# Performance work log

Hardware: AMD Instinct MI355X
Metric: run time of the kernel (lower is better)

## Reference

```python
import math
import jax, jax.numpy as jnp
import numpy as np

K = 4            # ensemble size
S_CONST = 0.25   # isotropic gaussian scale constant
GAUSS_DIM = 6

def pixel_shuffle(x, r):
    B, C, H, W = x.shape
    C2 = C // (r * r)
    x = x.reshape(B, C2, r, r, H, W).transpose(0, 1, 4, 2, 5, 3)
    return x.reshape(B, C2, H * r, W * r)

def pixel_unshuffle(x, r):
    B, C, H, W = x.shape
    x = x.reshape(B, C, H // r, r, W // r, r).transpose(0, 1, 3, 5, 2, 4)
    return x.reshape(B, C * r * r, H // r, W // r)

def setup_inputs():
    key = jax.random.key(0)
    k1, k2, k3 = jax.random.split(key, 3)
    B, h, w = 4, 128, 128
    inp = jax.random.normal(k1, (B, 3, h, w), jnp.float32)
    w_enc = jax.random.normal(k2, (1024, 3, 3, 3), jnp.float32) * 0.05
    b_enc = jnp.zeros((1024,), jnp.float32)
    w_head = jax.random.normal(k3, (GAUSS_DIM * K, 256), jnp.float32) * 0.05
    b_head = jnp.zeros((GAUSS_DIM * K,), jnp.float32)
    return {"inp": inp, "w_enc": w_enc, "b_enc": b_enc,
            "w_head": w_head, "b_head": b_head, "scale": 2}

def _forward(inp, w_enc, b_enc, w_head, b_head, scale):
    B, _, h, w = inp.shape
    s1 = s2 = float(scale)
    H, W = round(h * s1), round(w * s2)
    # --- encoder (conv3x3 -> pixel_shuffle x4 -> 64ch @ 4h x 4w) ---
    x = jax.lax.conv_general_dilated(inp, w_enc, (1, 1), 'SAME',
        dimension_numbers=('NCHW', 'OIHW', 'NCHW')) + b_enc[None, :, None, None]
    x = pixel_shuffle(x, 4)                 # [B, 64, 4h, 4w]
    feat = pixel_unshuffle(x, 2)            # [B, 256, 2h, 2w]
    # --- gauss head (1x1 conv) ---
    pred_map = jnp.einsum('bchw,oc->bohw', feat, w_head) + b_head[None, :, None, None]
    gh, gw = 2 * h, 2 * w
    N = gh * gw
    pred = pred_map.reshape(B, GAUSS_DIM * K, N).transpose(0, 2, 1).reshape(B, N, K, GAUSS_DIM)
    rgb_k, off_raw, w_logits = pred[..., :3], pred[..., 3:5], pred[..., 5:6]
    wgt = jax.nn.softmax(w_logits, axis=2)
    rgb = (rgb_k * wgt).sum(2)              # [B, N, 3]
    off = (jnp.tanh(off_raw) * wgt).sum(2)  # [B, N, 2]
    # --- gaussian centers in NDC ---
    yi, xi = jnp.meshgrid(jnp.arange(gh), jnp.arange(gw), indexing='ij')
    coordx = (xi / gw * 2.0 - 1.0).reshape(-1).astype(jnp.float32)
    coordy = (yi / gh * 2.0 - 1.0).reshape(-1).astype(jnp.float32)
    x_ndc = coordx[None, :] + 2.0 * off[..., 0] / w - 1.0 / W
    y_ndc = coordy[None, :] + 2.0 * off[..., 1] / h - 1.0 / H
    # --- rasterize: isotropic gaussians, local 3-sigma window, scatter-add ---
    s_px = S_CONST * s1                     # pixel-space std (theta = 0)
    r = max(2, int(math.ceil(3.0 * s_px)))
    offs = jnp.arange(-r, r + 1)

    def raster_one(xn, yn, col):
        cx = 0.5 * ((xn + 1.0) * W - 1.0)   # ndc -> pixel center
        cy = 0.5 * ((yn + 1.0) * H - 1.0)
        px = jnp.floor(cx)[:, None] + offs  # [N, 2r+1]
        py = jnp.floor(cy)[:, None] + offs
        dx = px - cx[:, None]
        dy = py - cy[:, None]
        power = -0.5 * (dy[:, :, None] ** 2 + dx[:, None, :] ** 2) / (s_px * s_px)
        alpha = jnp.minimum(0.999, jnp.exp(power))
        alpha = jnp.where(alpha > 1.0 / 255.0, alpha, 0.0)   # kernel alpha cutoff
        pxi = px.astype(jnp.int32)
        pyi = py.astype(jnp.int32)
        valid = ((pyi[:, :, None] >= 0) & (pyi[:, :, None] < H) &
                 (pxi[:, None, :] >= 0) & (pxi[:, None, :] < W))
        contrib = jnp.where(valid, alpha, 0.0)               # [N, wy, wx]
        yfull = jnp.clip(jnp.broadcast_to(pyi[:, :, None], contrib.shape), 0, H - 1)
        xfull = jnp.clip(jnp.broadcast_to(pxi[:, None, :], contrib.shape), 0, W - 1)
        img = jnp.zeros((H, W, 3), jnp.float32).at[yfull, xfull].add(
            contrib[..., None] * col[:, None, None, :])
        return jnp.clip(img, 0.0, 1.0).transpose(2, 0, 1)    # [3, H, W]

    return jax.vmap(raster_one)(x_ndc, y_ndc, rgb)

def reference(inp, w_enc, b_enc, w_head, b_head, scale):
    return _forward(inp, w_enc, b_enc, w_head, b_head, scale)
```

## Files before the change

### kernel.cpp

```cpp
#include <hip/hip_runtime.h>
#include <math.h>

#define NB 4
#define IH 128
#define IW 128
#define GH 256
#define GW 256
#define NGAUSS (NB * GH * GW)

#define WEFF_FLOATS (4 * 24 * 27)
#define BEFF_FLOATS (4 * 24)
#define POS_OFF 2688
#define COL_OFF (POS_OFF + 2 * NGAUSS)

#define TSX 16
#define TSY 16
#define GR 22
#define NREG (GR * GR)
#define RR_MAX 2.770360f
#define EXP2C (-2.8853900818f)

__device__ __forceinline__ float fast_tanh(float x) {
  return 1.f - 2.f / (__expf(2.f * x) + 1.f);
}
__device__ __forceinline__ float clamp01(float v) {
  return fminf(1.f, fmaxf(0.f, v));
}

__global__ __launch_bounds__(256) void weff_kernel(
    const float* __restrict__ w_enc, const float* __restrict__ b_enc,
    const float* __restrict__ w_head, const float* __restrict__ b_head,
    float* __restrict__ weff, float* __restrict__ beff) {
  __shared__ float sWH[24 * 256];
  __shared__ float sWE[256 * 27];
  __shared__ float sBE[256];

  int tid = (int)threadIdx.x;
  int p = (int)blockIdx.x;
  int ph = p >> 1, pw = p & 1;

  for (int i = tid; i < 24 * 256; i += 256) sWH[i] = w_head[i];
  {
    int hc = tid;
    int ch = ((hc >> 2) << 4) + (2 * ph + ((hc >> 1) & 1)) * 4 + (2 * pw + (hc & 1));
    for (int t = 0; t < 27; ++t) sWE[hc * 27 + t] = w_enc[ch * 27 + t];
    sBE[hc] = b_enc[ch];
  }
  __syncthreads();

  for (int j = tid; j < 24 * 27; j += 256) {
    int o = j / 27, t = j % 27;
    float a = 0.f;
    for (int hc = 0; hc < 256; ++hc) a = fmaf(sWH[o * 256 + hc], sWE[hc * 27 + t], a);
    weff[p * (24 * 27) + j] = a;
  }
  if (tid < 24) {
    float a = b_head[tid];
    for (int hc = 0; hc < 256; ++hc) a = fmaf(sWH[tid * 256 + hc], sBE[hc], a);
    beff[p * 24 + tid] = a;
  }
}

__global__ __launch_bounds__(256, 4) void gauss_kernel(
    const float* __restrict__ inp, const float* __restrict__ ws_ro,
    float* __restrict__ ws) {
  __shared__ float sW[4 * 24 * 28];
  __shared__ float sB[BEFF_FLOATS];

  int tid = (int)threadIdx.x;
  for (int i = tid; i < 4 * 24 * 28; i += 256) {
    int row = i / 28, k = i - row * 28;
    sW[i] = (k < 27) ? ws_ro[row * 27 + k] : 0.f;
  }
  for (int i = tid; i < BEFF_FLOATS; i += 256) sB[i] = ws_ro[WEFF_FLOATS + i];
  __syncthreads();

  int bid = (int)blockIdx.x;
  int b = bid >> 8;
  int t = bid & 255;
  int hh = (t >> 4) * 16 + (tid >> 4);
  int ww = (t & 15) * 16 + (tid & 15);
  int p = (hh & 1) * 2 + (ww & 1);
  int hs = hh >> 1, ws_ = ww >> 1;

  const float* ib = inp + b * 3 * IH * IW;
  float in[28];
  in[27] = 0.f;
  #pragma unroll
  for (int cin = 0; cin < 3; ++cin) {
    #pragma unroll
    for (int ky = 0; ky < 3; ++ky) {
      int y = hs + ky - 1;
      bool yok = (y >= 0 && y < IH);
      #pragma unroll
      for (int kx = 0; kx < 3; ++kx) {
        int x = ws_ + kx - 1;
        float v = 0.f;
        if (yok && x >= 0 && x < IW) v = ib[(cin * IH + y) * IW + x];
        in[cin * 9 + ky * 3 + kx] = v;
      }
    }
  }

  float pr[24];
  #pragma unroll
  for (int o = 0; o < 24; ++o) {
    float a = sB[p * 24 + o];
    const float4* wrow = (const float4*)&sW[(p * 24 + o) * 28];
    #pragma unroll
    for (int kq = 0; kq < 7; ++kq) {
      float4 w = wrow[kq];
      a = fmaf(in[kq * 4 + 0], w.x, a);
      a = fmaf(in[kq * 4 + 1], w.y, a);
      a = fmaf(in[kq * 4 + 2], w.z, a);
      a = fmaf(in[kq * 4 + 3], w.w, a);
    }
    pr[o] = a;
  }

  float l0 = pr[5], l1 = pr[11], l2 = pr[17], l3 = pr[23];
  float m = fmaxf(fmaxf(l0, l1), fmaxf(l2, l3));
  float e0 = __expf(l0 - m), e1 = __expf(l1 - m);
  float e2 = __expf(l2 - m), e3 = __expf(l3 - m);
  float inv = 1.f / (e0 + e1 + e2 + e3);
  float w0 = e0 * inv, w1 = e1 * inv, w2 = e2 * inv, w3 = e3 * inv;
  float cr = w0 * pr[0] + w1 * pr[6] + w2 * pr[12] + w3 * pr[18];
  float cg = w0 * pr[1] + w1 * pr[7] + w2 * pr[13] + w3 * pr[19];
  float cb = w0 * pr[2] + w1 * pr[8] + w2 * pr[14] + w3 * pr[20];
  float ox = w0 * fast_tanh(pr[3]) + w1 * fast_tanh(pr[9]) +
             w2 * fast_tanh(pr[15]) + w3 * fast_tanh(pr[21]);
  float oy = w0 * fast_tanh(pr[4]) + w1 * fast_tanh(pr[10]) +
             w2 * fast_tanh(pr[16]) + w3 * fast_tanh(pr[22]);

  float coordx = ((float)ww / 256.f) * 2.f - 1.f;
  float coordy = ((float)hh / 256.f) * 2.f - 1.f;
  float x_ndc = coordx + 2.f * ox / 128.f - 1.f / 256.f;
  float y_ndc = coordy + 2.f * oy / 128.f - 1.f / 256.f;
  float cx = 0.5f * ((x_ndc + 1.f) * 256.f - 1.f);
  float cy = 0.5f * ((y_ndc + 1.f) * 256.f - 1.f);

  int g = (b << 16) | (hh << 8) | ww;
  ((float2*)(ws + POS_OFF))[g] = make_float2(cy, cx);
  ((float4*)(ws + COL_OFF))[g] = make_float4(cr, cg, cb, 0.f);
}

__global__ __launch_bounds__(256, 4) void gather_kernel(
    const float* __restrict__ ws, float* __restrict__ out) {
  __shared__ float2 sPos[NREG];
  __shared__ float4 sCol[NREG];

  int tid = (int)threadIdx.x;
  int bid = (int)blockIdx.x;
  int b = bid >> 8;
  int t = bid & 255;
  int TY = (t >> 4) * TSY;
  int TX = (t & 15) * TSX;
  const float2* posP = (const float2*)(ws + POS_OFF);
  const float4* colP = (const float4*)(ws + COL_OFF);

  for (int i = tid; i < NREG; i += 256) {
    int r = i / GR, c = i - r * GR;
    int hh = TY - 2 + r, ww = TX - 2 + c;
    if ((unsigned)hh < GH && (unsigned)ww < GW) {
      int g = (b << 16) | (hh << 8) | ww;
      sPos[i] = posP[g];
      sCol[i] = colP[g];
    } else {
      sPos[i] = make_float2(1e9f, 1e9f);
      sCol[i] = make_float4(0.f, 0.f, 0.f, 0.f);
    }
  }
  __syncthreads();

  int pxl = tid & 15, pyl = tid >> 4;
  float fpx = (float)(TX + pxl), fpy = (float)(TY + pyl);
  float ar = 0.f, ag = 0.f, ab = 0.f;

  #pragma unroll
  for (int ry = 0; ry < 7; ++ry) {
    int base = (pyl + ry) * GR + pxl;
    #pragma unroll
    for (int rx = 0; rx < 7; ++rx) {
      float2 P = sPos[base + rx];
      float dy = fpy - P.x;
      float dx = fpx - P.y;
      float rr = fmaf(dy, dy, dx * dx);
      if (rr < RR_MAX) {
        float al = fminf(0.999f, exp2f(EXP2C * rr));
        float4 C = sCol[base + rx];
        ar = fmaf(al, C.x, ar);
        ag = fmaf(al, C.y, ag);
        ab = fmaf(al, C.z, ab);
      }
    }
  }

  float* ob = out + b * 3 * GH * GW;
  int i0 = (TY + pyl) * GW + (TX + pxl);
  ob[i0] = clamp01(ar);
  ob[GH * GW + i0] = clamp01(ag);
  ob[2 * GH * GW + i0] = clamp01(ab);
}

extern "C" void kernel_launch(void* const* d_in, const int* in_sizes, int n_in,
                              void* d_out, int out_size, void* d_ws, size_t ws_size,
                              hipStream_t stream) {
  const float* inp = (const float*)d_in[0];
  const float* w_enc = (const float*)d_in[1];
  const float* b_enc = (const float*)d_in[2];
  const float* w_head = (const float*)d_in[3];
  const float* b_head = (const float*)d_in[4];

  float* ws = (float*)d_ws;
  float* weff = ws;
  float* beff = ws + WEFF_FLOATS;

  weff_kernel<<<4, 256, 0, stream>>>(w_enc, b_enc, w_head, b_head, weff, beff);

  gauss_kernel<<<NB * 256, 256, 0, stream>>>(inp, ws, ws);

  gather_kernel<<<NB * 256, 256, 0, stream>>>(ws, (float*)d_out);
}
```

Baseline: 112.9 us.

## Fuse gaussian prediction into rasterization kernel with halo recomputation

Merges the per-pixel gaussian parameter kernel into the gather/raster kernel. Each tile stages its input patch in shared memory and recomputes the gaussians for its 22x22 halo region directly into shared memory, one parity class per wave. This removes the global workspace round trip for positions and colors and one kernel launch. In exchange it roughly doubles the gaussian compute through halo recomputation, and lanes are partly idle in the second iteration.

```diff
diff --git a/kernel.cpp b/kernel.cpp
--- a/kernel.cpp
+++ b/kernel.cpp
@@ -6,12 +6,9 @@
 #define IW 128
 #define GH 256
 #define GW 256
-#define NGAUSS (NB * GH * GW)
 
 #define WEFF_FLOATS (4 * 24 * 27)
 #define BEFF_FLOATS (4 * 24)
-#define POS_OFF 2688
-#define COL_OFF (POS_OFF + 2 * NGAUSS)
 
 #define TSX 16
 #define TSY 16
@@ -19,6 +16,9 @@
 #define NREG (GR * GR)
 #define RR_MAX 2.770360f
 #define EXP2C (-2.8853900818f)
+
+#define IPS 13
+#define IPSP 14
 
 __device__ __forceinline__ float fast_tanh(float x) {
   return 1.f - 2.f / (__expf(2.f * x) + 1.f);
@@ -61,91 +61,12 @@
   }
 }
 
-__global__ __launch_bounds__(256, 4) void gauss_kernel(
+__global__ __launch_bounds__(256, 4) void render_kernel(
     const float* __restrict__ inp, const float* __restrict__ ws_ro,
-    float* __restrict__ ws) {
+    float* __restrict__ out) {
   __shared__ float sW[4 * 24 * 28];
   __shared__ float sB[BEFF_FLOATS];
-
-  int tid = (int)threadIdx.x;
-  for (int i = tid; i < 4 * 24 * 28; i += 256) {
-    int row = i / 28, k = i - row * 28;
-    sW[i] = (k < 27) ? ws_ro[row * 27 + k] : 0.f;
-  }
-  for (int i = tid; i < BEFF_FLOATS; i += 256) sB[i] = ws_ro[WEFF_FLOATS + i];
-  __syncthreads();
-
-  int bid = (int)blockIdx.x;
-  int b = bid >> 8;
-  int t = bid & 255;
-  int hh = (t >> 4) * 16 + (tid >> 4);
-  int ww = (t & 15) * 16 + (tid & 15);
-  int p = (hh & 1) * 2 + (ww & 1);
-  int hs = hh >> 1, ws_ = ww >> 1;
-
-  const float* ib = inp + b * 3 * IH * IW;
-  float in[28];
-  in[27] = 0.f;
-  #pragma unroll
-  for (int cin = 0; cin < 3; ++cin) {
-    #pragma unroll
-    for (int ky = 0; ky < 3; ++ky) {
-      int y = hs + ky - 1;
-      bool yok = (y >= 0 && y < IH);
-      #pragma unroll
-      for (int kx = 0; kx < 3; ++kx) {
-        int x = ws_ + kx - 1;
-        float v = 0.f;
-        if (yok && x >= 0 && x < IW) v = ib[(cin * IH + y) * IW + x];
-        in[cin * 9 + ky * 3 + kx] = v;
-      }
-    }
-  }
-
-  float pr[24];
-  #pragma unroll
-  for (int o = 0; o < 24; ++o) {
-    float a = sB[p * 24 + o];
-    const float4* wrow = (const float4*)&sW[(p * 24 + o) * 28];
-    #pragma unroll
-    for (int kq = 0; kq < 7; ++kq) {
-      float4 w = wrow[kq];
-      a = fmaf(in[kq * 4 + 0], w.x, a);
-      a = fmaf(in[kq * 4 + 1], w.y, a);
-      a = fmaf(in[kq * 4 + 2], w.z, a);
-      a = fmaf(in[kq * 4 + 3], w.w, a);
-    }
-    pr[o] = a;
-  }
-
-  float l0 = pr[5], l1 = pr[11], l2 = pr[17], l3 = pr[23];
-  float m = fmaxf(fmaxf(l0, l1), fmaxf(l2, l3));
-  float e0 = __expf(l0 - m), e1 = __expf(l1 - m);
-  float e2 = __expf(l2 - m), e3 = __expf(l3 - m);
-  float inv = 1.f / (e0 + e1 + e2 + e3);
-  float w0 = e0 * inv, w1 = e1 * inv, w2 = e2 * inv, w3 = e3 * inv;
-  float cr = w0 * pr[0] + w1 * pr[6] + w2 * pr[12] + w3 * pr[18];
-  float cg = w0 * pr[1] + w1 * pr[7] + w2 * pr[13] + w3 * pr[19];
-  float cb = w0 * pr[2] + w1 * pr[8] + w2 * pr[14] + w3 * pr[20];
-  float ox = w0 * fast_tanh(pr[3]) + w1 * fast_tanh(pr[9]) +
-             w2 * fast_tanh(pr[15]) + w3 * fast_tanh(pr[21]);
-  float oy = w0 * fast_tanh(pr[4]) + w1 * fast_tanh(pr[10]) +
-             w2 * fast_tanh(pr[16]) + w3 * fast_tanh(pr[22]);
-
-  float coordx = ((float)ww / 256.f) * 2.f - 1.f;
-  float coordy = ((float)hh / 256.f) * 2.f - 1.f;
-  float x_ndc = coordx + 2.f * ox / 128.f - 1.f / 256.f;
-  float y_ndc = coordy + 2.f * oy / 128.f - 1.f / 256.f;
-  float cx = 0.5f * ((x_ndc + 1.f) * 256.f - 1.f);
-  float cy = 0.5f * ((y_ndc + 1.f) * 256.f - 1.f);
-
-  int g = (b << 16) | (hh << 8) | ww;
-  ((float2*)(ws + POS_OFF))[g] = make_float2(cy, cx);
-  ((float4*)(ws + COL_OFF))[g] = make_float4(cr, cg, cb, 0.f);
-}
-
-__global__ __launch_bounds__(256, 4) void gather_kernel(
-    const float* __restrict__ ws, float* __restrict__ out) {
+  __shared__ float sIn[3 * IPS * IPSP];
   __shared__ float2 sPos[NREG];
   __shared__ float4 sCol[NREG];
 
@@ -155,19 +76,97 @@
   int t = bid & 255;
   int TY = (t >> 4) * TSY;
   int TX = (t & 15) * TSX;
-  const float2* posP = (const float2*)(ws + POS_OFF);
-  const float4* colP = (const float4*)(ws + COL_OFF);
-
-  for (int i = tid; i < NREG; i += 256) {
-    int r = i / GR, c = i - r * GR;
-    int hh = TY - 2 + r, ww = TX - 2 + c;
-    if ((unsigned)hh < GH && (unsigned)ww < GW) {
-      int g = (b << 16) | (hh << 8) | ww;
-      sPos[i] = posP[g];
-      sCol[i] = colP[g];
-    } else {
-      sPos[i] = make_float2(1e9f, 1e9f);
-      sCol[i] = make_float4(0.f, 0.f, 0.f, 0.f);
+
+  for (int i = tid; i < 4 * 24 * 28; i += 256) {
+    int row = i / 28, k = i - row * 28;
+    sW[i] = (k < 27) ? ws_ro[row * 27 + k] : 0.f;
+  }
+  for (int i = tid; i < BEFF_FLOATS; i += 256) sB[i] = ws_ro[WEFF_FLOATS + i];
+
+  {
+    const float* ib = inp + b * 3 * IH * IW;
+    int y0 = (TY >> 1) - 2, x0 = (TX >> 1) - 2;
+    for (int i = tid; i < 3 * IPS * IPSP; i += 256) {
+      int c = i / (IPS * IPSP);
+      int r = i - c * (IPS * IPSP);
+      int ry = r / IPSP, rx = r - ry * IPSP;
+      float v = 0.f;
+      int y = y0 + ry, x = x0 + rx;
+      if (rx < IPS && y >= 0 && y < IH && x >= 0 && x < IW)
+        v = ib[(c * IH + y) * IW + x];
+      sIn[i] = v;
+    }
+  }
+  __syncthreads();
+
+  {
+    int wave = tid >> 6;
+    int lane = tid & 63;
+    int ph = wave >> 1, pw = wave & 1;
+    for (int j = lane; j < 121; j += 64) {
+      int qy = j / 11, qx = j - qy * 11;
+      int gyr = 2 * qy + ph, gxr = 2 * qx + pw;
+      int gi = gyr * GR + gxr;
+      int hh = TY - 2 + gyr, ww = TX - 2 + gxr;
+
+      if ((unsigned)hh < GH && (unsigned)ww < GW) {
+        float in[28];
+        in[27] = 0.f;
+        #pragma unroll
+        for (int cin = 0; cin < 3; ++cin) {
+          #pragma unroll
+          for (int ky = 0; ky < 3; ++ky) {
+            int rr_ = (qy + ky) * IPSP + qx;
+            #pragma unroll
+            for (int kx = 0; kx < 3; ++kx) {
+              in[cin * 9 + ky * 3 + kx] = sIn[cin * IPS * IPSP + rr_ + kx];
+            }
+          }
+        }
+
+        float pr[24];
+        #pragma unroll
+        for (int o = 0; o < 24; ++o) {
+          float a = sB[wave * 24 + o];
+          const float4* wrow = (const float4*)&sW[(wave * 24 + o) * 28];
+          #pragma unroll
+          for (int kq = 0; kq < 7; ++kq) {
+            float4 w = wrow[kq];
+            a = fmaf(in[kq * 4 + 0], w.x, a);
+            a = fmaf(in[kq * 4 + 1], w.y, a);
+            a = fmaf(in[kq * 4 + 2], w.z, a);
+            a = fmaf(in[kq * 4 + 3], w.w, a);
+          }
+          pr[o] = a;
+        }
+
+        float l0 = pr[5], l1 = pr[11], l2 = pr[17], l3 = pr[23];
+        float m = fmaxf(fmaxf(l0, l1), fmaxf(l2, l3));
+        float e0 = __expf(l0 - m), e1 = __expf(l1 - m);
+        float e2 = __expf(l2 - m), e3 = __expf(l3 - m);
+        float inv = 1.f / (e0 + e1 + e2 + e3);
+        float w0 = e0 * inv, w1 = e1 * inv, w2 = e2 * inv, w3 = e3 * inv;
+        float cr = w0 * pr[0] + w1 * pr[6] + w2 * pr[12] + w3 * pr[18];
+        float cg = w0 * pr[1] + w1 * pr[7] + w2 * pr[13] + w3 * pr[19];
+        float cb = w0 * pr[2] + w1 * pr[8] + w2 * pr[14] + w3 * pr[20];
+        float ox = w0 * fast_tanh(pr[3]) + w1 * fast_tanh(pr[9]) +
+                   w2 * fast_tanh(pr[15]) + w3 * fast_tanh(pr[21]);
+        float oy = w0 * fast_tanh(pr[4]) + w1 * fast_tanh(pr[10]) +
+                   w2 * fast_tanh(pr[16]) + w3 * fast_tanh(pr[22]);
+
+        float coordx = ((float)ww / 256.f) * 2.f - 1.f;
+        float coordy = ((float)hh / 256.f) * 2.f - 1.f;
+        float x_ndc = coordx + 2.f * ox / 128.f - 1.f / 256.f;
+        float y_ndc = coordy + 2.f * oy / 128.f - 1.f / 256.f;
+        float cx = 0.5f * ((x_ndc + 1.f) * 256.f - 1.f);
+        float cy = 0.5f * ((y_ndc + 1.f) * 256.f - 1.f);
+
+        sPos[gi] = make_float2(cy, cx);
+        sCol[gi] = make_float4(cr, cg, cb, 0.f);
+      } else {
+        sPos[gi] = make_float2(1e9f, 1e9f);
+        sCol[gi] = make_float4(0.f, 0.f, 0.f, 0.f);
+      }
     }
   }
   __syncthreads();
@@ -217,7 +216,5 @@
 
   weff_kernel<<<4, 256, 0, stream>>>(w_enc, b_enc, w_head, b_head, weff, beff);
 
-  gauss_kernel<<<NB * 256, 256, 0, stream>>>(inp, ws, ws);
-
-  gather_kernel<<<NB * 256, 256, 0, stream>>>(ws, (float*)d_out);
-}
+  render_kernel<<<NB * 256, 256, 0, stream>>>(inp, ws, (float*)d_out);
+}
```

New measurement: 106.5 us. -5.6%, faster.
